# Performance work log

Measured on AMD Instinct MI355X. Metric: run time of the kernel, lower is better.

Reference implementation:

```python
import jax, jax.numpy as jnp
import numpy as np

SCALES = (3, 5, 7)

def _avg_pool3d_same(x, k):
    # stride-1 avg_pool3d with padding k//2, count_include_pad=True (torch default).
    # For odd k <= dim this preserves the spatial size, so the subsequent
    # F.interpolate to the input size is an exact identity.
    p = k // 2
    s = jax.lax.reduce_window(
        x, 0.0, jax.lax.add,
        window_dimensions=(1, 1, k, k, k),
        window_strides=(1, 1, 1, 1, 1),
        padding=[(0, 0), (0, 0), (p, p), (p, p), (p, p)])
    return s * (1.0 / float(k ** 3))

def setup_inputs() -> dict:
    key = jax.random.key(0)
    k1, k2 = jax.random.split(key)
    B, C, D, H, W = 2, 48, 64, 64, 64
    x = jax.random.normal(k1, (B, C, D, H, W), dtype=jnp.float32)
    fuse_w = jax.random.normal(k2, (1, len(SCALES) * C), dtype=jnp.float32) * 0.05
    fuse_b = jnp.zeros((1,), dtype=jnp.float32)
    return {"x": x, "fuse_w": fuse_w, "fuse_b": fuse_b}

def reference(x, fuse_w, fuse_b):
    # Multi-scale stride-1 average pooling (sizes preserved -> interp is identity)
    pooled = [_avg_pool3d_same(x, k) for k in SCALES]   # each (B, C, D, H, W)
    cat = jnp.concatenate(pooled, axis=1)               # (B, 3C, D, H, W)
    # 1x1x1 conv to a single channel, then sigmoid
    out = jnp.einsum('bcdhw,oc->bodhw', cat, fuse_w) + fuse_b[None, :, None, None, None]
    return jax.nn.sigmoid(out)                          # (B, 1, D, H, W)
```

## Files before the change

### kernel.cpp

```cpp
#include <hip/hip_runtime.h>
#include <math.h>

#define CH       48
#define DIM      64
#define SPATIAL  (DIM * DIM * DIM)
#define NB       2
#define VOL      (NB * SPATIAL)
#define NSCALES  3

__global__ __launch_bounds__(256) void k_chanred(
        const float* __restrict__ x,
        const float* __restrict__ fw,
        float* __restrict__ z) {
    __shared__ float sw[NSCALES * CH];
    if (threadIdx.x < NSCALES * CH) sw[threadIdx.x] = fw[threadIdx.x];
    __syncthreads();

    int gid = blockIdx.x * blockDim.x + threadIdx.x;
    int b   = gid >> 16;
    int sp4 = gid & 0xFFFF;

    const float4* xb = (const float4*)x + (size_t)b * (CH * (SPATIAL / 4)) + sp4;

    float4 a0 = make_float4(0.f, 0.f, 0.f, 0.f);
    float4 a1 = make_float4(0.f, 0.f, 0.f, 0.f);
    float4 a2 = make_float4(0.f, 0.f, 0.f, 0.f);

    #pragma unroll 4
    for (int c = 0; c < CH; ++c) {
        float4 v = xb[(size_t)c * (SPATIAL / 4)];
        float w0 = sw[c], w1 = sw[CH + c], w2 = sw[2 * CH + c];
        a0.x += w0 * v.x; a0.y += w0 * v.y; a0.z += w0 * v.z; a0.w += w0 * v.w;
        a1.x += w1 * v.x; a1.y += w1 * v.y; a1.z += w1 * v.z; a1.w += w1 * v.w;
        a2.x += w2 * v.x; a2.y += w2 * v.y; a2.z += w2 * v.z; a2.w += w2 * v.w;
    }

    float4* z4 = (float4*)z;
    size_t o = (size_t)b * (SPATIAL / 4) + sp4;
    z4[o]                 = a0;
    z4[(VOL / 4) + o]     = a1;
    z4[2 * (VOL / 4) + o] = a2;
}

__global__ __launch_bounds__(256) void k_poolw(
        const float* __restrict__ in, float* __restrict__ out) {
    int gid = blockIdx.x * blockDim.x + threadIdx.x;
    int s   = gid >> 19;
    int w0  = gid & 63;
    int p   = s + 1;
    const float* row = in + (gid - w0);
    int lo = w0 - p; if (lo < 0)  lo = 0;
    int hi = w0 + p; if (hi > 63) hi = 63;
    float acc = 0.f;
    for (int w = lo; w <= hi; ++w) acc += row[w];
    out[gid] = acc;
}

__global__ __launch_bounds__(256) void k_poolh(
        const float* __restrict__ in, float* __restrict__ out) {
    int gid = blockIdx.x * blockDim.x + threadIdx.x;
    int s   = gid >> 19;
    int h0  = (gid >> 6) & 63;
    int p   = s + 1;
    const float* col = in + (gid - (h0 << 6));
    int lo = h0 - p; if (lo < 0)  lo = 0;
    int hi = h0 + p; if (hi > 63) hi = 63;
    float acc = 0.f;
    for (int h = lo; h <= hi; ++h) acc += col[h << 6];
    out[gid] = acc;
}

__global__ __launch_bounds__(256) void k_poold_fuse(
        const float* __restrict__ in,
        const float* __restrict__ fb,
        float* __restrict__ out) {
    int gid = blockIdx.x * blockDim.x + threadIdx.x;
    int d0  = (gid >> 12) & 63;

    const float inv[NSCALES] = {1.f / 27.f, 1.f / 125.f, 1.f / 343.f};
    float acc = fb[0];

    #pragma unroll
    for (int s = 0; s < NSCALES; ++s) {
        int p  = s + 1;
        int lo = d0 - p; if (lo < 0)  lo = 0;
        int hi = d0 + p; if (hi > 63) hi = 63;
        const float* base = in + (size_t)s * VOL + (gid - (d0 << 12));
        float a = 0.f;
        for (int d = lo; d <= hi; ++d) a += base[d << 12];
        acc += a * inv[s];
    }
    out[gid] = 1.f / (1.f + __expf(-acc));
}

extern "C" void kernel_launch(void* const* d_in, const int* in_sizes, int n_in,
                              void* d_out, int out_size, void* d_ws, size_t ws_size,
                              hipStream_t stream) {
    const float* x  = (const float*)d_in[0];
    const float* fw = (const float*)d_in[1];
    const float* fb = (const float*)d_in[2];
    float* out = (float*)d_out;

    float* ws0 = (float*)d_ws;
    float* ws1 = ws0 + (size_t)NSCALES * VOL;

    k_chanred<<<(VOL / 4) / 256, 256, 0, stream>>>(x, fw, ws0);
    k_poolw<<<(NSCALES * VOL) / 256, 256, 0, stream>>>(ws0, ws1);
    k_poolh<<<(NSCALES * VOL) / 256, 256, 0, stream>>>(ws1, ws0);
    k_poold_fuse<<<VOL / 256, 256, 0, stream>>>(ws0, fb, out);
}
```

Baseline: 38.57 us.

## Fuse W-axis pooling into channel reduction and vectorize H/D pooling passes

```diff
diff --git a/kernel.cpp b/kernel.cpp
--- a/kernel.cpp
+++ b/kernel.cpp
@@ -6,68 +6,81 @@
 #define SPATIAL  (DIM * DIM * DIM)
 #define NB       2
 #define VOL      (NB * SPATIAL)
-#define NSCALES  3
+#define NS       3
+#define ROWS     16
 
-__global__ __launch_bounds__(256) void k_chanred(
+typedef float f4 __attribute__((ext_vector_type(4)));
+
+__global__ __launch_bounds__(256) void k_chanred_wpool(
         const float* __restrict__ x,
         const float* __restrict__ fw,
         float* __restrict__ z) {
-    __shared__ float sw[NSCALES * CH];
-    if (threadIdx.x < NSCALES * CH) sw[threadIdx.x] = fw[threadIdx.x];
+    __shared__ float sw[NS * CH];
+    __shared__ f4 tile[NS][ROWS][16];
+    const int tid = threadIdx.x;
+    if (tid < NS * CH) sw[tid] = fw[tid];
     __syncthreads();
 
-    int gid = blockIdx.x * blockDim.x + threadIdx.x;
-    int b   = gid >> 16;
-    int sp4 = gid & 0xFFFF;
+    const int lr  = tid >> 4;
+    const int lw  = tid & 15;
+    const int row = blockIdx.x * ROWS + lr;
+    const int b   = row >> 12;
 
-    const float4* xb = (const float4*)x + (size_t)b * (CH * (SPATIAL / 4)) + sp4;
+    const f4* xp = (const f4*)x
+        + (size_t)b * CH * (SPATIAL / 4)
+        + (size_t)(row & 4095) * 16 + lw;
 
-    float4 a0 = make_float4(0.f, 0.f, 0.f, 0.f);
-    float4 a1 = make_float4(0.f, 0.f, 0.f, 0.f);
-    float4 a2 = make_float4(0.f, 0.f, 0.f, 0.f);
+    f4 a0 = {0,0,0,0}, a1 = {0,0,0,0}, a2 = {0,0,0,0};
+    #pragma unroll 8
+    for (int c = 0; c < CH; ++c) {
+        f4 v = __builtin_nontemporal_load(&xp[(size_t)c * (SPATIAL / 4)]);
+        a0 += sw[c] * v;
+        a1 += sw[CH + c] * v;
+        a2 += sw[2 * CH + c] * v;
+    }
+    tile[0][lr][lw] = a0;
+    tile[1][lr][lw] = a1;
+    tile[2][lr][lw] = a2;
+    __syncthreads();
 
-    #pragma unroll 4
-    for (int c = 0; c < CH; ++c) {
-        float4 v = xb[(size_t)c * (SPATIAL / 4)];
-        float w0 = sw[c], w1 = sw[CH + c], w2 = sw[2 * CH + c];
-        a0.x += w0 * v.x; a0.y += w0 * v.y; a0.z += w0 * v.z; a0.w += w0 * v.w;
-        a1.x += w1 * v.x; a1.y += w1 * v.y; a1.z += w1 * v.z; a1.w += w1 * v.w;
-        a2.x += w2 * v.x; a2.y += w2 * v.y; a2.z += w2 * v.z; a2.w += w2 * v.w;
+    f4* z4 = (f4*)z;
+    const size_t ob = (size_t)row * 16 + lw;
+    const f4 zero = {0,0,0,0};
+    #pragma unroll
+    for (int s = 0; s < NS; ++s) {
+        f4 m1 = (lw > 0)  ? tile[s][lr][lw - 1] : zero;
+        f4 m0 = tile[s][lr][lw];
+        f4 p1 = (lw < 15) ? tile[s][lr][lw + 1] : zero;
+        float f[12] = {m1.x, m1.y, m1.z, m1.w,
+                       m0.x, m0.y, m0.z, m0.w,
+                       p1.x, p1.y, p1.z, p1.w};
+        const int p = s + 1;
+        f4 r;
+        #pragma unroll
+        for (int j = 0; j < 4; ++j) {
+            float acc = 0.f;
+            #pragma unroll
+            for (int i = -3; i <= 3; ++i)
+                if (i >= -p && i <= p) acc += f[4 + j + i];
+            r[j] = acc;
+        }
+        z4[(size_t)s * (VOL / 4) + ob] = r;
     }
-
-    float4* z4 = (float4*)z;
-    size_t o = (size_t)b * (SPATIAL / 4) + sp4;
-    z4[o]                 = a0;
-    z4[(VOL / 4) + o]     = a1;
-    z4[2 * (VOL / 4) + o] = a2;
-}
-
-__global__ __launch_bounds__(256) void k_poolw(
-        const float* __restrict__ in, float* __restrict__ out) {
-    int gid = blockIdx.x * blockDim.x + threadIdx.x;
-    int s   = gid >> 19;
-    int w0  = gid & 63;
-    int p   = s + 1;
-    const float* row = in + (gid - w0);
-    int lo = w0 - p; if (lo < 0)  lo = 0;
-    int hi = w0 + p; if (hi > 63) hi = 63;
-    float acc = 0.f;
-    for (int w = lo; w <= hi; ++w) acc += row[w];
-    out[gid] = acc;
 }
 
 __global__ __launch_bounds__(256) void k_poolh(
         const float* __restrict__ in, float* __restrict__ out) {
     int gid = blockIdx.x * blockDim.x + threadIdx.x;
-    int s   = gid >> 19;
-    int h0  = (gid >> 6) & 63;
+    int s   = gid >> 17;
+    int r   = gid & 0x1FFFF;
+    int h   = (r >> 4) & 63;
     int p   = s + 1;
-    const float* col = in + (gid - (h0 << 6));
-    int lo = h0 - p; if (lo < 0)  lo = 0;
-    int hi = h0 + p; if (hi > 63) hi = 63;
-    float acc = 0.f;
-    for (int h = lo; h <= hi; ++h) acc += col[h << 6];
-    out[gid] = acc;
+    const f4* col = (const f4*)in + ((size_t)s << 17) + (r - (h << 4));
+    int lo = h - p; if (lo < 0)  lo = 0;
+    int hi = h + p; if (hi > 63) hi = 63;
+    f4 a = {0,0,0,0};
+    for (int hh = lo; hh <= hi; ++hh) a += col[hh << 4];
+    ((f4*)out)[gid] = a;
 }
 
 __global__ __launch_bounds__(256) void k_poold_fuse(
@@ -75,22 +88,25 @@
         const float* __restrict__ fb,
         float* __restrict__ out) {
     int gid = blockIdx.x * blockDim.x + threadIdx.x;
-    int d0  = (gid >> 12) & 63;
-
-    const float inv[NSCALES] = {1.f / 27.f, 1.f / 125.f, 1.f / 343.f};
-    float acc = fb[0];
-
+    int d   = (gid >> 10) & 63;
+    int base = gid - (d << 10);
+    const float inv[NS] = {1.f / 27.f, 1.f / 125.f, 1.f / 343.f};
+    const float bias = fb[0];
+    f4 acc = {bias, bias, bias, bias};
     #pragma unroll
-    for (int s = 0; s < NSCALES; ++s) {
+    for (int s = 0; s < NS; ++s) {
         int p  = s + 1;
-        int lo = d0 - p; if (lo < 0)  lo = 0;
-        int hi = d0 + p; if (hi > 63) hi = 63;
-        const float* base = in + (size_t)s * VOL + (gid - (d0 << 12));
-        float a = 0.f;
-        for (int d = lo; d <= hi; ++d) a += base[d << 12];
+        int lo = d - p; if (lo < 0)  lo = 0;
+        int hi = d + p; if (hi > 63) hi = 63;
+        const f4* bp = (const f4*)in + ((size_t)s << 17) + base;
+        f4 a = {0,0,0,0};
+        for (int dd = lo; dd <= hi; ++dd) a += bp[dd << 10];
         acc += a * inv[s];
     }
-    out[gid] = 1.f / (1.f + __expf(-acc));
+    f4 r;
+    #pragma unroll
+    for (int j = 0; j < 4; ++j) r[j] = 1.f / (1.f + __expf(-acc[j]));
+    __builtin_nontemporal_store(r, &((f4*)out)[gid]);
 }
 
 extern "C" void kernel_launch(void* const* d_in, const int* in_sizes, int n_in,
@@ -102,10 +118,9 @@
     float* out = (float*)d_out;
 
     float* ws0 = (float*)d_ws;
-    float* ws1 = ws0 + (size_t)NSCALES * VOL;
+    float* ws1 = ws0 + (size_t)NS * VOL;
 
-    k_chanred<<<(VOL / 4) / 256, 256, 0, stream>>>(x, fw, ws0);
-    k_poolw<<<(NSCALES * VOL) / 256, 256, 0, stream>>>(ws0, ws1);
-    k_poolh<<<(NSCALES * VOL) / 256, 256, 0, stream>>>(ws1, ws0);
-    k_poold_fuse<<<VOL / 256, 256, 0, stream>>>(ws0, fb, out);
+    k_chanred_wpool<<<(NB * DIM * DIM) / ROWS, 256, 0, stream>>>(x, fw, ws0);
+    k_poolh<<<(NS * VOL / 4) / 256, 256, 0, stream>>>(ws0, ws1);
+    k_poold_fuse<<<(VOL / 4) / 256, 256, 0, stream>>>(ws1, fb, out);
 }
```

After: 32.84 us. -14.9%, faster.
